# Kernel optimization log

Hardware: AMD Instinct MI355X
Metric: run time of the kernel (lower is better)

The kernel has to match this reference:

```python
import jax, jax.numpy as jnp
import numpy as np

H, W = 32, 64          # img_size
NB = 4                 # fno_blocks
SCALE = 0.02


def setup_inputs() -> dict:
    key = jax.random.key(0)
    ks = jax.random.split(key, 8)
    B, N, C = 16, H * W, 768
    BS = C // NB
    x = jax.random.normal(ks[0], (B, N, C), dtype=jnp.float32)
    w1 = SCALE * jax.random.normal(ks[1], (2, NB, BS, BS), dtype=jnp.float32)
    b1 = SCALE * jax.random.normal(ks[2], (2, NB, BS), dtype=jnp.float32)
    w2 = SCALE * jax.random.normal(ks[3], (2, NB, BS, BS), dtype=jnp.float32)
    b2 = SCALE * jax.random.normal(ks[4], (2, NB, BS), dtype=jnp.float32)
    # Conv1d(C, C, kernel_size=1) == per-token linear layer over channels
    bias_w = jax.random.normal(ks[5], (C, C), dtype=jnp.float32) / np.sqrt(C)
    bias_b = jax.random.normal(ks[6], (C,), dtype=jnp.float32) * 0.01
    return {"x": x, "w1": w1, "b1": b1, "w2": w2, "b2": b2,
            "bias_w": bias_w, "bias_b": bias_b}


def _mul(a, w):
    # block-diagonal matmul: a [..., NB, BS], w [NB, BS, BS]
    return jnp.einsum('...bd,bdk->...bk', a, w)


def reference(x, w1, b1, w2, b2, bias_w, bias_b):
    B, N, C = x.shape
    BS = C // NB
    # Conv1d kernel-size-1 bias path
    bias = x @ bias_w.T + bias_b
    # spatial FFT
    xf = jnp.fft.rfftn(x.reshape(B, H, W, C), axes=(1, 2), norm='ortho')
    xf = xf.reshape(B, H, W // 2 + 1, NB, BS)
    xr, xi = xf.real, xf.imag
    # layer 1 (complex block-diag matmul + bias, ReLU on real/imag separately)
    r1 = jax.nn.relu(_mul(xr, w1[0]) - _mul(xi, w1[1]) + b1[0])
    i1 = jax.nn.relu(_mul(xr, w1[1]) + _mul(xi, w1[0]) + b1[1])
    # layer 2 -- NOTE: imag part uses the *updated* real part, matching the
    # original torch code's in-place reassignment order.
    r2 = _mul(r1, w2[0]) - _mul(i1, w2[1]) + b2[0]
    i2 = _mul(r2, w2[1]) + _mul(i1, w2[0]) + b2[1]
    xc = jax.lax.complex(r2, i2).reshape(B, H, W // 2 + 1, C)
    out = jnp.fft.irfftn(xc, s=(H, W), axes=(1, 2), norm='ortho')
    return out.reshape(B, N, C) + bias
```

## Files before the change

kernel.cpp:

```cpp
#include <hip/hip_runtime.h>
#include <hip/hip_bf16.h>
#include <stdint.h>

#define BB 16
#define HH 32
#define WW 64
#define CC 768
#define W2C 33
#define ROWW (2*CC)

typedef __bf16 bf16x8 __attribute__((ext_vector_type(8)));
typedef float f32x4 __attribute__((ext_vector_type(4)));

__device__ __forceinline__ unsigned short f2bf(float f) {
  __hip_bfloat16 h = __float2bfloat16(f);
  return __builtin_bit_cast(unsigned short, h);
}
__device__ __forceinline__ float bf2f(unsigned short u) {
  union { unsigned int i; float f; } x;
  x.i = ((unsigned int)u) << 16;
  return x.f;
}

__device__ __forceinline__ void g2l16(const void* g, void* l) {
  __builtin_amdgcn_global_load_lds((const __attribute__((address_space(1))) unsigned int*)g,
                                   (__attribute__((address_space(3))) unsigned int*)l,
                                   16, 0, 0);
}

#define WAITVM(n) asm volatile("s_waitcnt vmcnt(" #n ")" ::: "memory")
#define LGKM0() asm volatile("s_waitcnt lgkmcnt(0)" ::: "memory")
#define MEMFENCE() asm volatile("" ::: "memory")

__device__ __host__ constexpr int brevc(int x, int bits) {
  int r = 0;
  for (int i = 0; i < bits; ++i) r |= ((x >> i) & 1) << (bits - 1 - i);
  return r;
}

constexpr double TPI = 6.283185307179586476925286766559;
constexpr double tsin_(double x) {
  double t = x, s = x, x2 = x * x;
  for (int i = 1; i < 14; ++i) { t *= -x2 / (double)((2 * i) * (2 * i + 1)); s += t; }
  return s;
}
constexpr double tcos_(double x) {
  double t = 1.0, s = 1.0, x2 = x * x;
  for (int i = 1; i < 14; ++i) { t *= -x2 / (double)((2 * i - 1) * (2 * i)); s += t; }
  return s;
}
struct Tw64 { float c[64]; float s[64]; };
constexpr Tw64 mk_tw() {
  Tw64 r{};
  for (int k = 0; k < 64; ++k) {
    int q = k >> 4, m = k & 15;
    double a = (TPI / 64.0) * m;
    double cq = tcos_(a), sq = tsin_(a);
    double c, s;
    if (q == 0)      { c =  cq; s =  sq; }
    else if (q == 1) { c = -sq; s =  cq; }
    else if (q == 2) { c = -cq; s = -sq; }
    else             { c =  sq; s = -cq; }
    r.c[k] = (float)c;
    r.s[k] = (float)(-s);
  }
  return r;
}
constexpr Tw64 TW = mk_tw();

template<int N, bool INV>
__device__ __forceinline__ void fft_reg(float2 (&v)[N]) {
  constexpr int LOG2N = (N == 64) ? 6 : 5;
#pragma unroll
  for (int s = 0; s < LOG2N; ++s) {
    const int len = N >> s;
    const int half = len >> 1;
    const int tstep = 64 / len;
#pragma unroll
    for (int i = 0; i < N; i += len) {
#pragma unroll
      for (int j = 0; j < half; ++j) {
        float2 u = v[i + j];
        float2 t = v[i + j + half];
        float sr = u.x + t.x, si = u.y + t.y;
        float dr = u.x - t.x, di = u.y - t.y;
        float wr = TW.c[j * tstep];
        float wi = INV ? -TW.s[j * tstep] : TW.s[j * tstep];
        v[i + j] = make_float2(sr, si);
        v[i + j + half] = make_float2(dr * wr - di * wi, dr * wi + di * wr);
      }
    }
  }
}

__global__ __launch_bounds__(128) void fft_fwd_w(const float* __restrict__ x,
                                                 ushort2* __restrict__ yw) {
  __shared__ __align__(16) float xs[32][128];
  const int t = threadIdx.x;
  const int bh = blockIdx.x;
  const int c0 = blockIdx.y * 128;
  const float* xrow = x + (size_t)bh * (WW * CC) + c0;
  const int rg = t >> 5;
  const int lc = (t & 31) * 4;
  float2 v[32];
#pragma unroll
  for (int half = 0; half < 2; ++half) {
    if (half) __syncthreads();
    float4 f[8];
#pragma unroll
    for (int it = 0; it < 8; ++it)
      f[it] = *(const float4*)(xrow + (size_t)(half * 32 + it * 4 + rg) * CC + lc);
#pragma unroll
    for (int it = 0; it < 8; ++it)
      *(float4*)&xs[it * 4 + rg][lc] = f[it];
    __syncthreads();
#pragma unroll
    for (int n = 0; n < 16; ++n)
      v[half * 16 + n] = make_float2(xs[2 * n][t], xs[2 * n + 1][t]);
  }
  fft_reg<32, false>(v);
  ushort2* yp = yw + (size_t)bh * (W2C * CC) + c0 + t;
  {
    float2 Z0 = v[0];
    yp[0] = make_ushort2(f2bf(Z0.x + Z0.y), f2bf(0.f));
    yp[(size_t)32 * CC] = make_ushort2(f2bf(Z0.x - Z0.y), f2bf(0.f));
  }
#pragma unroll
  for (int k = 1; k < 32; ++k) {
    float2 Zk = v[brevc(k, 5)];
    float2 Zm = v[brevc(32 - k, 5)];
    float Er = 0.5f * (Zk.x + Zm.x), Ei = 0.5f * (Zk.y - Zm.y);
    float Odr = 0.5f * (Zk.y + Zm.y), Odi = -0.5f * (Zk.x - Zm.x);
    float wx = TW.c[k], wy = TW.s[k];
    float Xr = Er + wx * Odr - wy * Odi;
    float Xi = Ei + wx * Odi + wy * Odr;
    yp[(size_t)k * CC] = make_ushort2(f2bf(Xr), f2bf(Xi));
  }
}

__global__ __launch_bounds__(256) void fft_fwd_h(const ushort2* __restrict__ yw,
                                                 unsigned short* __restrict__ xf) {
  const int bk = blockIdx.x;
  const int b = bk / W2C, kw = bk - b * W2C;
  const int c = blockIdx.y * 256 + threadIdx.x;
  const ushort2* yp = yw + ((size_t)b * HH * W2C + kw) * CC + c;
  float2 v[32];
#pragma unroll
  for (int h = 0; h < 32; ++h) {
    ushort2 u = yp[(size_t)h * (W2C * CC)];
    v[h] = make_float2(bf2f(u.x), bf2f(u.y));
  }
  fft_reg<32, false>(v);
  const int nb = c / 192, cc = c - nb * 192;
  ushort2* xp = (ushort2*)(xf + (size_t)nb * 384 + 2 * cc);
  const float s = 0.022097086912079608f;
#pragma unroll
  for (int kh = 0; kh < 32; ++kh) {
    float2 z = v[brevc(kh, 5)];
    size_t m = ((size_t)b * HH + kh) * W2C + kw;
    xp[m * (ROWW / 2)] = make_ushort2(f2bf(z.x * s), f2bf(z.y * s));
  }
}

__global__ __launch_bounds__(256) void fft_inv_h(const unsigned short* __restrict__ r2,
                                                 ushort2* __restrict__ g) {
  const int bk = blockIdx.x;
  const int b = bk / W2C, kw = bk - b * W2C;
  const int c = blockIdx.y * 256 + threadIdx.x;
  const int nb = c / 192, cc = c - nb * 192;
  const ushort2* rp = (const ushort2*)(r2 + (size_t)nb * 384 + 2 * cc);
  float2 v[32];
#pragma unroll
  for (int kh = 0; kh < 32; ++kh) {
    size_t m = ((size_t)b * HH + kh) * W2C + kw;
    ushort2 u = rp[m * (ROWW / 2)];
    v[kh] = make_float2(bf2f(u.x), bf2f(u.y));
  }
  fft_reg<32, true>(v);
  ushort2* gp = g + ((size_t)b * HH * W2C + kw) * CC + c;
#pragma unroll
  for (int h = 0; h < 32; ++h) {
    float2 z = v[brevc(h, 5)];
    gp[(size_t)h * (W2C * CC)] = make_ushort2(f2bf(z.x), f2bf(z.y));
  }
}

__global__ __launch_bounds__(128) void fft_inv_w(const ushort2* __restrict__ g,
                                                 const unsigned short* __restrict__ biasb,
                                                 float* __restrict__ out) {
  __shared__ __align__(16) float ys[32][128];
  const int t = threadIdx.x;
  const int bh = blockIdx.x;
  const int c0 = blockIdx.y * 128;
  const ushort2* gp = g + (size_t)bh * (W2C * CC) + c0 + t;
  float2 v[32];
  {
    float X0 = bf2f(gp[0].x);
    float X32 = bf2f(gp[(size_t)32 * CC].x);
    v[0] = make_float2(0.5f * (X0 + X32), 0.5f * (X0 - X32));
  }
#pragma unroll
  for (int k = 1; k < 32; ++k) {
    ushort2 uk = gp[(size_t)k * CC];
    ushort2 um = gp[(size_t)(32 - k) * CC];
    float2 Xk = make_float2(bf2f(uk.x), bf2f(uk.y));
    float2 Xm = make_float2(bf2f(um.x), bf2f(um.y));
    float Ar = 0.5f * (Xk.x + Xm.x), Ai = 0.5f * (Xk.y - Xm.y);
    float Dr = 0.5f * (Xk.x - Xm.x), Di = 0.5f * (Xk.y + Xm.y);
    float wx = TW.c[k], wy = TW.s[k];
    float Br = wx * Dr + wy * Di;
    float Bi = wx * Di - wy * Dr;
    v[k] = make_float2(Ar - Bi, Ai + Br);
  }
  fft_reg<32, true>(v);
  const float s2 = 0.04419417382415922f;
  float* orow = out + (size_t)bh * (WW * CC) + c0;
  const unsigned short* brow = biasb + (size_t)bh * (WW * CC) + c0;
  const int rg = t >> 5;
  const int lc = (t & 31) * 4;
#pragma unroll
  for (int half = 0; half < 2; ++half) {
    if (half) __syncthreads();
    ushort4 b4[8];
#pragma unroll
    for (int it = 0; it < 8; ++it)
      b4[it] = *(const ushort4*)(brow + (size_t)(half * 32 + it * 4 + rg) * CC + lc);
#pragma unroll
    for (int n = 0; n < 16; ++n) {
      float2 z = v[brevc(half * 16 + n, 5)];
      ys[2 * n][t] = z.x * s2;
      ys[2 * n + 1][t] = z.y * s2;
    }
    __syncthreads();
#pragma unroll
    for (int it = 0; it < 8; ++it) {
      const int w = half * 32 + it * 4 + rg;
      float4 f = *(const float4*)&ys[it * 4 + rg][lc];
      f.x += bf2f(b4[it].x); f.y += bf2f(b4[it].y);
      f.z += bf2f(b4[it].z); f.w += bf2f(b4[it].w);
      *(float4*)(orow + (size_t)w * CC + lc) = f;
    }
  }
}

template<bool RELU, bool OBF>
__global__ __launch_bounds__(256) void gemm_bt(
    const unsigned short* __restrict__ A, int lda, int aZ,
    const unsigned short* __restrict__ Bw, int K, int bZ,
    const float* __restrict__ bias, int biasZ,
    void* __restrict__ outp, int ldo, int oZ) {
  __shared__ __align__(16) unsigned short As[2][128 * 32];
  __shared__ __align__(16) unsigned short Bs[2][128 * 32];
  const int t = threadIdx.x;
  const int z = blockIdx.z;
  const size_t m0 = (size_t)blockIdx.x * 128;
  const int n0 = blockIdx.y * 128;
  const unsigned short* Ap = A + m0 * lda + (size_t)z * aZ;
  const unsigned short* Bp = Bw + (size_t)n0 * K + (size_t)z * bZ;
  const int lane = t & 63, wave = t >> 6;
  const int lr = lane & 15, quad = lane >> 4;
  const int wm = (wave >> 1) * 64, wn = (wave & 1) * 64;
  const int row = t >> 2;
  const int sl = t & 3;
  const int kb = (sl ^ ((row >> 1) & 3)) * 8;
  const int swzf = (lr >> 1) & 3;
  const int NT = K >> 5;
  f32x4 acc[4][4] = {};

#define STG(k0_, s_) do { \
    const unsigned short* ga_ = Ap + (size_t)row * lda + ((k0_) + kb); \
    g2l16(ga_, &As[s_][row * 32 + sl * 8]); \
    g2l16(ga_ + (size_t)64 * lda, &As[s_][(row + 64) * 32 + sl * 8]); \
    const unsigned short* gb_ = Bp + (size_t)row * K + ((k0_) + kb); \
    g2l16(gb_, &Bs[s_][row * 32 + sl * 8]); \
    g2l16(gb_ + (size_t)64 * K, &Bs[s_][(row + 64) * 32 + sl * 8]); \
  } while (0)

  STG(0, 0);
  WAITVM(0);
  MEMFENCE(); __builtin_amdgcn_s_barrier(); MEMFENCE();
  int cur = 0;
  for (int tt = 0; tt < NT; ++tt) {
    if (tt + 1 < NT) STG((tt + 1) * 32, cur ^ 1);
    bf16x8 af[4], bfr[4];
#pragma unroll
    for (int mi = 0; mi < 4; ++mi)
      af[mi] = *(const bf16x8*)&As[cur][(wm + mi * 16 + lr) * 32 + ((quad ^ swzf) * 8)];
#pragma unroll
    for (int ni = 0; ni < 4; ++ni)
      bfr[ni] = *(const bf16x8*)&Bs[cur][(wn + ni * 16 + lr) * 32 + ((quad ^ swzf) * 8)];
    __builtin_amdgcn_s_setprio(1);
#pragma unroll
    for (int mi = 0; mi < 4; ++mi)
#pragma unroll
      for (int ni = 0; ni < 4; ++ni)
        acc[mi][ni] = __builtin_amdgcn_mfma_f32_16x16x32_bf16(af[mi], bfr[ni], acc[mi][ni], 0, 0, 0);
    __builtin_amdgcn_s_setprio(0);
    if (tt + 1 < NT) {
      WAITVM(0);
      MEMFENCE(); __builtin_amdgcn_s_barrier(); MEMFENCE();
      cur ^= 1;
    }
  }
#undef STG

#pragma unroll
  for (int mi = 0; mi < 4; ++mi) {
    const size_t mrow = m0 + wm + mi * 16 + quad * 4;
#pragma unroll
    for (int ni = 0; ni < 4; ++ni) {
      const int ncol = n0 + wn + ni * 16 + lr;
      const float bv = bias[z * biasZ + ncol];
#pragma unroll
      for (int r = 0; r < 4; ++r) {
        float vv = acc[mi][ni][r] + bv;
        if (RELU) vv = fmaxf(vv, 0.f);
        const size_t off = (mrow + r) * (size_t)ldo + (size_t)z * oZ + ncol;
        if (OBF) ((unsigned short*)outp)[off] = f2bf(vv);
        else ((float*)outp)[off] = vv;
      }
    }
  }
}

__global__ __launch_bounds__(256) void gemm_bias(
    const float* __restrict__ A,
    const unsigned short* __restrict__ Bw,
    const float* __restrict__ bias,
    unsigned short* __restrict__ outp) {
  constexpr int K = 768, NT = 24, LDAF = 768;
  __shared__ __align__(16) unsigned short As[2][128 * 32];
  __shared__ __align__(16) unsigned short Bs[2][128 * 32];
  const int t = threadIdx.x;
  const size_t m0 = (size_t)blockIdx.x * 128;
  const int n0 = blockIdx.y * 128;
  const float* Ap = A + m0 * LDAF;
  const unsigned short* Bp = Bw + (size_t)n0 * K;
  const int lane = t & 63, wave = t >> 6;
  const int lr = lane & 15, quad = lane >> 4;
  const int wm = (wave >> 1) * 64, wn = (wave & 1) * 64;
  const int row = t >> 2, sl = t & 3;
  const int kb = (sl ^ ((row >> 1) & 3)) * 8;
  const int swzf = (lr >> 1) & 3;
  f32x4 acc[4][4] = {};
  float4 a0, a1, a2, a3;

#define LDA4(k0_) do { \
    const float* ga_ = Ap + (size_t)row * LDAF + ((k0_) + kb); \
    a0 = *(const float4*)ga_; a1 = *(const float4*)(ga_ + 4); \
    const float* gc_ = ga_ + (size_t)64 * LDAF; \
    a2 = *(const float4*)gc_; a3 = *(const float4*)(gc_ + 4); \
  } while (0)
#define STB(k0_, s_) do { \
    const unsigned short* gb_ = Bp + (size_t)row * K + ((k0_) + kb); \
    g2l16(gb_, &Bs[s_][row * 32 + sl * 8]); \
    g2l16(gb_ + (size_t)64 * K, &Bs[s_][(row + 64) * 32 + sl * 8]); \
  } while (0)
#define WRA(s_) do { \
    union { bf16x8 v; unsigned short u[8]; } p0_, p1_; \
    p0_.u[0] = f2bf(a0.x); p0_.u[1] = f2bf(a0.y); p0_.u[2] = f2bf(a0.z); p0_.u[3] = f2bf(a0.w); \
    p0_.u[4] = f2bf(a1.x); p0_.u[5] = f2bf(a1.y); p0_.u[6] = f2bf(a1.z); p0_.u[7] = f2bf(a1.w); \
    p1_.u[0] = f2bf(a2.x); p1_.u[1] = f2bf(a2.y); p1_.u[2] = f2bf(a2.z); p1_.u[3] = f2bf(a2.w); \
    p1_.u[4] = f2bf(a3.x); p1_.u[5] = f2bf(a3.y); p1_.u[6] = f2bf(a3.z); p1_.u[7] = f2bf(a3.w); \
    *(bf16x8*)&As[s_][row * 32 + sl * 8] = p0_.v; \
    *(bf16x8*)&As[s_][(row + 64) * 32 + sl * 8] = p1_.v; \
  } while (0)

  LDA4(0); STB(0, 0);
  WRA(0);
  WAITVM(0); LGKM0();
  MEMFENCE(); __builtin_amdgcn_s_barrier(); MEMFENCE();
  int cur = 0;
  for (int tt = 0; tt < NT; ++tt) {
    if (tt + 1 < NT) { LDA4((tt + 1) * 32); STB((tt + 1) * 32, cur ^ 1); }
    bf16x8 af[4], bfr[4];
#pragma unroll
    for (int mi = 0; mi < 4; ++mi)
      af[mi] = *(const bf16x8*)&As[cur][(wm + mi * 16 + lr) * 32 + ((quad ^ swzf) * 8)];
#pragma unroll
    for (int ni = 0; ni < 4; ++ni)
      bfr[ni] = *(const bf16x8*)&Bs[cur][(wn + ni * 16 + lr) * 32 + ((quad ^ swzf) * 8)];
    __builtin_amdgcn_s_setprio(1);
#pragma unroll
    for (int mi = 0; mi < 4; ++mi)
#pragma unroll
      for (int ni = 0; ni < 4; ++ni)
        acc[mi][ni] = __builtin_amdgcn_mfma_f32_16x16x32_bf16(af[mi], bfr[ni], acc[mi][ni], 0, 0, 0);
    __builtin_amdgcn_s_setprio(0);
    if (tt + 1 < NT) {
      WRA(cur ^ 1);
      WAITVM(0); LGKM0();
      MEMFENCE(); __builtin_amdgcn_s_barrier(); MEMFENCE();
      cur ^= 1;
    }
  }
#undef LDA4
#undef STB
#undef WRA

#pragma unroll
  for (int mi = 0; mi < 4; ++mi) {
    const size_t mrow = m0 + wm + mi * 16 + quad * 4;
#pragma unroll
    for (int ni = 0; ni < 4; ++ni) {
      const int ncol = n0 + wn + ni * 16 + lr;
      const float bv = bias[ncol];
#pragma unroll
      for (int r = 0; r < 4; ++r)
        outp[(mrow + r) * (size_t)768 + ncol] = f2bf(acc[mi][ni][r] + bv);
    }
  }
}

__global__ __launch_bounds__(256) void cvt_bf16(const float* __restrict__ in,
                                                unsigned short* __restrict__ outp) {
  const size_t i = ((size_t)blockIdx.x * 256 + threadIdx.x) * 4;
  float4 v = *(const float4*)(in + i);
  ushort4 o = make_ushort4(f2bf(v.x), f2bf(v.y), f2bf(v.z), f2bf(v.w));
  *(ushort4*)(outp + i) = o;
}

__global__ __launch_bounds__(256) void build_w1(const float* __restrict__ w1,
                                                const float* __restrict__ b1,
                                                unsigned short* __restrict__ w1t,
                                                float* __restrict__ bias1) {
  const int idx = blockIdx.x * 256 + threadIdx.x;
  const int nb = idx / (384 * 384);
  const int rem = idx - nb * (384 * 384);
  const int n = rem / 384, k = rem - (rem / 384) * 384;
  const bool khi = k >= 192, nhi = n >= 192;
  const int kk = khi ? k - 192 : k, nn = nhi ? n - 192 : n;
  float val;
  if (!khi && !nhi)      val =  w1[((0 * 4 + nb) * 192 + kk) * 192 + nn];
  else if (khi && !nhi)  val = -w1[((1 * 4 + nb) * 192 + kk) * 192 + nn];
  else if (!khi && nhi)  val =  w1[((1 * 4 + nb) * 192 + kk) * 192 + nn];
  else                   val =  w1[((0 * 4 + nb) * 192 + kk) * 192 + nn];
  const int k2 = 2 * kk + (khi ? 1 : 0);
  const int n2 = 2 * nn + (nhi ? 1 : 0);
  w1t[((size_t)nb * 384 + n2) * 384 + k2] = f2bf(val);
  if (k == 0)
    bias1[nb * 384 + n2] = nhi ? b1[(1 * 4 + nb) * 192 + nn] : b1[(0 * 4 + nb) * 192 + nn];
}

__global__ __launch_bounds__(256) void build_w2(const float* __restrict__ w2,
                                                const float* __restrict__ b2,
                                                unsigned short* __restrict__ w2t,
                                                float* __restrict__ bias2) {
  const int idx = blockIdx.x * 256 + threadIdx.x;
  const int nb = idx / (384 * 384);
  const int rem = idx - nb * (384 * 384);
  const int k = rem / 384, n = rem - (rem / 384) * 384;
  const bool khi = k >= 192, nhi = n >= 192;
  const int kk = khi ? k - 192 : k, nn = nhi ? n - 192 : n;
  float val;
  if (!khi && !nhi) {
    val = w2[((0 * 4 + nb) * 192 + kk) * 192 + nn];
  } else if (khi && !nhi) {
    val = -w2[((1 * 4 + nb) * 192 + kk) * 192 + nn];
  } else if (!khi && nhi) {
    float s = 0.f;
    for (int d = 0; d < 192; ++d)
      s += w2[((0 * 4 + nb) * 192 + kk) * 192 + d] * w2[((1 * 4 + nb) * 192 + d) * 192 + nn];
    val = s;
  } else {
    float s = 0.f;
    for (int d = 0; d < 192; ++d)
      s += w2[((1 * 4 + nb) * 192 + kk) * 192 + d] * w2[((1 * 4 + nb) * 192 + d) * 192 + nn];
    val = w2[((0 * 4 + nb) * 192 + kk) * 192 + nn] - s;
  }
  const int k2 = 2 * kk + (khi ? 1 : 0);
  const int n2 = 2 * nn + (nhi ? 1 : 0);
  w2t[((size_t)nb * 384 + n2) * 384 + k2] = f2bf(val);
  if (k == 0) {
    float bv;
    if (!nhi) {
      bv = b2[(0 * 4 + nb) * 192 + nn];
    } else {
      float s = 0.f;
      for (int d = 0; d < 192; ++d)
        s += b2[(0 * 4 + nb) * 192 + d] * w2[((1 * 4 + nb) * 192 + d) * 192 + nn];
      bv = b2[(1 * 4 + nb) * 192 + nn] + s;
    }
    bias2[nb * 384 + n2] = bv;
  }
}

extern "C" void kernel_launch(void* const* d_in, const int* in_sizes, int n_in,
                              void* d_out, int out_size, void* d_ws, size_t ws_size,
                              hipStream_t stream) {
  (void)in_sizes; (void)n_in; (void)out_size; (void)ws_size;
  const float* x  = (const float*)d_in[0];
  const float* w1 = (const float*)d_in[1];
  const float* b1 = (const float*)d_in[2];
  const float* w2 = (const float*)d_in[3];
  const float* b2 = (const float*)d_in[4];
  const float* bw = (const float*)d_in[5];
  const float* bb = (const float*)d_in[6];
  float* out = (float*)d_out;

  char* p = (char*)d_ws;
  unsigned short* buf1 = (unsigned short*)p; p += 51904512;
  unsigned short* buf2 = (unsigned short*)p; p += 51904512;
  unsigned short* buf3 = (unsigned short*)p; p += 51904512;
  unsigned short* bwb  = (unsigned short*)p; p += 1179648;
  unsigned short* w1t  = (unsigned short*)p; p += 1179648;
  unsigned short* w2t  = (unsigned short*)p; p += 1179648;
  float* bias1 = (float*)p; p += 6144;
  float* bias2 = (float*)p; p += 6144;

  cvt_bf16<<<589824 / 1024, 256, 0, stream>>>(bw, bwb);
  build_w1<<<589824 / 256, 256, 0, stream>>>(w1, b1, w1t, bias1);
  build_w2<<<589824 / 256, 256, 0, stream>>>(w2, b2, w2t, bias2);
  fft_fwd_w<<<dim3(BB * HH, 6), 128, 0, stream>>>(x, (ushort2*)buf1);
  gemm_bias<<<dim3(256, 6), 256, 0, stream>>>(x, bwb, bb, buf3);
  fft_fwd_h<<<dim3(BB * W2C, 3), 256, 0, stream>>>((const ushort2*)buf1, buf2);
  gemm_bt<true, true><<<dim3(132, 3, 4), 256, 0, stream>>>(
      buf2, ROWW, 384, w1t, 384, 384 * 384, bias1, 384, buf1, ROWW, 384);
  gemm_bt<false, true><<<dim3(132, 3, 4), 256, 0, stream>>>(
      buf1, ROWW, 384, w2t, 384, 384 * 384, bias2, 384, buf2, ROWW, 384);
  fft_inv_h<<<dim3(BB * W2C, 3), 256, 0, stream>>>(buf2, (ushort2*)buf1);
  fft_inv_w<<<dim3(BB * HH, 6), 128, 0, stream>>>((const ushort2*)buf1, buf3, out);
}
```

Before: 438.1 us.

## Merge weight prep kernels and co-schedule bias GEMM with forward H-FFT

The three weight-preparation kernels are merged into one launch that dispatches on block index. The bias-path GEMM and the forward H-direction FFT are combined into a single heterogeneous kernel that interleaves GEMM tiles with FFT blocks, so compute-bound MFMA work and memory-bound FFT work can share the GPU concurrently. This cuts launch count and inter-kernel gaps. In exchange the FFT blocks now reserve the GEMM's shared memory and register budget, which may lower their occupancy.

```diff
diff --git a/kernel.cpp b/kernel.cpp
--- a/kernel.cpp
+++ b/kernel.cpp
@@ -138,27 +138,121 @@
   }
 }
 
-__global__ __launch_bounds__(256) void fft_fwd_h(const ushort2* __restrict__ yw,
-                                                 unsigned short* __restrict__ xf) {
-  const int bk = blockIdx.x;
-  const int b = bk / W2C, kw = bk - b * W2C;
-  const int c = blockIdx.y * 256 + threadIdx.x;
-  const ushort2* yp = yw + ((size_t)b * HH * W2C + kw) * CC + c;
-  float2 v[32];
-#pragma unroll
-  for (int h = 0; h < 32; ++h) {
-    ushort2 u = yp[(size_t)h * (W2C * CC)];
-    v[h] = make_float2(bf2f(u.x), bf2f(u.y));
-  }
-  fft_reg<32, false>(v);
-  const int nb = c / 192, cc = c - nb * 192;
-  ushort2* xp = (ushort2*)(xf + (size_t)nb * 384 + 2 * cc);
-  const float s = 0.022097086912079608f;
-#pragma unroll
-  for (int kh = 0; kh < 32; ++kh) {
-    float2 z = v[brevc(kh, 5)];
-    size_t m = ((size_t)b * HH + kh) * W2C + kw;
-    xp[m * (ROWW / 2)] = make_ushort2(f2bf(z.x * s), f2bf(z.y * s));
+__global__ __launch_bounds__(256) void fused_bias_ffth(
+    const float* __restrict__ x, const unsigned short* __restrict__ bwb,
+    const float* __restrict__ bb, unsigned short* __restrict__ biasout,
+    const ushort2* __restrict__ yw, unsigned short* __restrict__ xf) {
+  __shared__ __align__(16) unsigned short As[2][128 * 32];
+  __shared__ __align__(16) unsigned short Bs[2][128 * 32];
+  const int gid = blockIdx.x;
+  bool isg; int idx;
+  if (gid < 3072) { isg = (gid & 1) == 0; idx = gid >> 1; }
+  else            { isg = false; idx = 1536 + (gid - 3072); }
+
+  if (isg) {
+    constexpr int K = 768, NT = 24, LDAF = 768;
+    const int t = threadIdx.x;
+    const int bx = idx & 255, by = idx >> 8;
+    const size_t m0 = (size_t)bx * 128;
+    const int n0 = by * 128;
+    const float* Ap = x + m0 * LDAF;
+    const unsigned short* Bp = bwb + (size_t)n0 * K;
+    const int lane = t & 63, wave = t >> 6;
+    const int lr = lane & 15, quad = lane >> 4;
+    const int wm = (wave >> 1) * 64, wn = (wave & 1) * 64;
+    const int row = t >> 2, sl = t & 3;
+    const int kb = (sl ^ ((row >> 1) & 3)) * 8;
+    const int swzf = (lr >> 1) & 3;
+    f32x4 acc[4][4] = {};
+    float4 a0, a1, a2, a3;
+
+#define LDA4(k0_) do { \
+    const float* ga_ = Ap + (size_t)row * LDAF + ((k0_) + kb); \
+    a0 = *(const float4*)ga_; a1 = *(const float4*)(ga_ + 4); \
+    const float* gc_ = ga_ + (size_t)64 * LDAF; \
+    a2 = *(const float4*)gc_; a3 = *(const float4*)(gc_ + 4); \
+  } while (0)
+#define STB(k0_, s_) do { \
+    const unsigned short* gb_ = Bp + (size_t)row * K + ((k0_) + kb); \
+    g2l16(gb_, &Bs[s_][row * 32 + sl * 8]); \
+    g2l16(gb_ + (size_t)64 * K, &Bs[s_][(row + 64) * 32 + sl * 8]); \
+  } while (0)
+#define WRA(s_) do { \
+    union { bf16x8 v; unsigned short u[8]; } p0_, p1_; \
+    p0_.u[0] = f2bf(a0.x); p0_.u[1] = f2bf(a0.y); p0_.u[2] = f2bf(a0.z); p0_.u[3] = f2bf(a0.w); \
+    p0_.u[4] = f2bf(a1.x); p0_.u[5] = f2bf(a1.y); p0_.u[6] = f2bf(a1.z); p0_.u[7] = f2bf(a1.w); \
+    p1_.u[0] = f2bf(a2.x); p1_.u[1] = f2bf(a2.y); p1_.u[2] = f2bf(a2.z); p1_.u[3] = f2bf(a2.w); \
+    p1_.u[4] = f2bf(a3.x); p1_.u[5] = f2bf(a3.y); p1_.u[6] = f2bf(a3.z); p1_.u[7] = f2bf(a3.w); \
+    *(bf16x8*)&As[s_][row * 32 + sl * 8] = p0_.v; \
+    *(bf16x8*)&As[s_][(row + 64) * 32 + sl * 8] = p1_.v; \
+  } while (0)
+
+    LDA4(0); STB(0, 0);
+    WRA(0);
+    WAITVM(0); LGKM0();
+    MEMFENCE(); __builtin_amdgcn_s_barrier(); MEMFENCE();
+    int cur = 0;
+    for (int tt = 0; tt < NT; ++tt) {
+      if (tt + 1 < NT) { LDA4((tt + 1) * 32); STB((tt + 1) * 32, cur ^ 1); }
+      bf16x8 af[4], bfr[4];
+#pragma unroll
+      for (int mi = 0; mi < 4; ++mi)
+        af[mi] = *(const bf16x8*)&As[cur][(wm + mi * 16 + lr) * 32 + ((quad ^ swzf) * 8)];
+#pragma unroll
+      for (int ni = 0; ni < 4; ++ni)
+        bfr[ni] = *(const bf16x8*)&Bs[cur][(wn + ni * 16 + lr) * 32 + ((quad ^ swzf) * 8)];
+      __builtin_amdgcn_s_setprio(1);
+#pragma unroll
+      for (int mi = 0; mi < 4; ++mi)
+#pragma unroll
+        for (int ni = 0; ni < 4; ++ni)
+          acc[mi][ni] = __builtin_amdgcn_mfma_f32_16x16x32_bf16(af[mi], bfr[ni], acc[mi][ni], 0, 0, 0);
+      __builtin_amdgcn_s_setprio(0);
+      if (tt + 1 < NT) {
+        WRA(cur ^ 1);
+        WAITVM(0); LGKM0();
+        MEMFENCE(); __builtin_amdgcn_s_barrier(); MEMFENCE();
+        cur ^= 1;
+      }
+    }
+#undef LDA4
+#undef STB
+#undef WRA
+
+#pragma unroll
+    for (int mi = 0; mi < 4; ++mi) {
+      const size_t mrow = m0 + wm + mi * 16 + quad * 4;
+#pragma unroll
+      for (int ni = 0; ni < 4; ++ni) {
+        const int ncol = n0 + wn + ni * 16 + lr;
+        const float bv = bb[ncol];
+#pragma unroll
+        for (int r = 0; r < 4; ++r)
+          biasout[(mrow + r) * (size_t)768 + ncol] = f2bf(acc[mi][ni][r] + bv);
+      }
+    }
+  } else {
+    const int bk = idx - (idx / 528) * 528;
+    const int cy = idx / 528;
+    const int b = bk / W2C, kw = bk - b * W2C;
+    const int c = cy * 256 + threadIdx.x;
+    const ushort2* yp = yw + ((size_t)b * HH * W2C + kw) * CC + c;
+    float2 v[32];
+#pragma unroll
+    for (int h = 0; h < 32; ++h) {
+      ushort2 u = yp[(size_t)h * (W2C * CC)];
+      v[h] = make_float2(bf2f(u.x), bf2f(u.y));
+    }
+    fft_reg<32, false>(v);
+    const int nb = c / 192, cc = c - nb * 192;
+    ushort2* xp = (ushort2*)(xf + (size_t)nb * 384 + 2 * cc);
+    const float s = 0.022097086912079608f;
+#pragma unroll
+    for (int kh = 0; kh < 32; ++kh) {
+      float2 z = v[brevc(kh, 5)];
+      size_t m = ((size_t)b * HH + kh) * W2C + kw;
+      xp[m * (ROWW / 2)] = make_ushort2(f2bf(z.x * s), f2bf(z.y * s));
+    }
   }
 }
 
@@ -323,165 +417,73 @@
   }
 }
 
-__global__ __launch_bounds__(256) void gemm_bias(
-    const float* __restrict__ A,
-    const unsigned short* __restrict__ Bw,
-    const float* __restrict__ bias,
-    unsigned short* __restrict__ outp) {
-  constexpr int K = 768, NT = 24, LDAF = 768;
-  __shared__ __align__(16) unsigned short As[2][128 * 32];
-  __shared__ __align__(16) unsigned short Bs[2][128 * 32];
+__global__ __launch_bounds__(256) void prep_all(
+    const float* __restrict__ bw, unsigned short* __restrict__ bwb,
+    const float* __restrict__ w1, const float* __restrict__ b1,
+    unsigned short* __restrict__ w1t, float* __restrict__ bias1,
+    const float* __restrict__ w2, const float* __restrict__ b2,
+    unsigned short* __restrict__ w2t, float* __restrict__ bias2) {
+  const int gid = blockIdx.x;
   const int t = threadIdx.x;
-  const size_t m0 = (size_t)blockIdx.x * 128;
-  const int n0 = blockIdx.y * 128;
-  const float* Ap = A + m0 * LDAF;
-  const unsigned short* Bp = Bw + (size_t)n0 * K;
-  const int lane = t & 63, wave = t >> 6;
-  const int lr = lane & 15, quad = lane >> 4;
-  const int wm = (wave >> 1) * 64, wn = (wave & 1) * 64;
-  const int row = t >> 2, sl = t & 3;
-  const int kb = (sl ^ ((row >> 1) & 3)) * 8;
-  const int swzf = (lr >> 1) & 3;
-  f32x4 acc[4][4] = {};
-  float4 a0, a1, a2, a3;
-
-#define LDA4(k0_) do { \
-    const float* ga_ = Ap + (size_t)row * LDAF + ((k0_) + kb); \
-    a0 = *(const float4*)ga_; a1 = *(const float4*)(ga_ + 4); \
-    const float* gc_ = ga_ + (size_t)64 * LDAF; \
-    a2 = *(const float4*)gc_; a3 = *(const float4*)(gc_ + 4); \
-  } while (0)
-#define STB(k0_, s_) do { \
-    const unsigned short* gb_ = Bp + (size_t)row * K + ((k0_) + kb); \
-    g2l16(gb_, &Bs[s_][row * 32 + sl * 8]); \
-    g2l16(gb_ + (size_t)64 * K, &Bs[s_][(row + 64) * 32 + sl * 8]); \
-  } while (0)
-#define WRA(s_) do { \
-    union { bf16x8 v; unsigned short u[8]; } p0_, p1_; \
-    p0_.u[0] = f2bf(a0.x); p0_.u[1] = f2bf(a0.y); p0_.u[2] = f2bf(a0.z); p0_.u[3] = f2bf(a0.w); \
-    p0_.u[4] = f2bf(a1.x); p0_.u[5] = f2bf(a1.y); p0_.u[6] = f2bf(a1.z); p0_.u[7] = f2bf(a1.w); \
-    p1_.u[0] = f2bf(a2.x); p1_.u[1] = f2bf(a2.y); p1_.u[2] = f2bf(a2.z); p1_.u[3] = f2bf(a2.w); \
-    p1_.u[4] = f2bf(a3.x); p1_.u[5] = f2bf(a3.y); p1_.u[6] = f2bf(a3.z); p1_.u[7] = f2bf(a3.w); \
-    *(bf16x8*)&As[s_][row * 32 + sl * 8] = p0_.v; \
-    *(bf16x8*)&As[s_][(row + 64) * 32 + sl * 8] = p1_.v; \
-  } while (0)
-
-  LDA4(0); STB(0, 0);
-  WRA(0);
-  WAITVM(0); LGKM0();
-  MEMFENCE(); __builtin_amdgcn_s_barrier(); MEMFENCE();
-  int cur = 0;
-  for (int tt = 0; tt < NT; ++tt) {
-    if (tt + 1 < NT) { LDA4((tt + 1) * 32); STB((tt + 1) * 32, cur ^ 1); }
-    bf16x8 af[4], bfr[4];
-#pragma unroll
-    for (int mi = 0; mi < 4; ++mi)
-      af[mi] = *(const bf16x8*)&As[cur][(wm + mi * 16 + lr) * 32 + ((quad ^ swzf) * 8)];
-#pragma unroll
-    for (int ni = 0; ni < 4; ++ni)
-      bfr[ni] = *(const bf16x8*)&Bs[cur][(wn + ni * 16 + lr) * 32 + ((quad ^ swzf) * 8)];
-    __builtin_amdgcn_s_setprio(1);
-#pragma unroll
-    for (int mi = 0; mi < 4; ++mi)
-#pragma unroll
-      for (int ni = 0; ni < 4; ++ni)
-        acc[mi][ni] = __builtin_amdgcn_mfma_f32_16x16x32_bf16(af[mi], bfr[ni], acc[mi][ni], 0, 0, 0);
-    __builtin_amdgcn_s_setprio(0);
-    if (tt + 1 < NT) {
-      WRA(cur ^ 1);
-      WAITVM(0); LGKM0();
-      MEMFENCE(); __builtin_amdgcn_s_barrier(); MEMFENCE();
-      cur ^= 1;
-    }
-  }
-#undef LDA4
-#undef STB
-#undef WRA
-
-#pragma unroll
-  for (int mi = 0; mi < 4; ++mi) {
-    const size_t mrow = m0 + wm + mi * 16 + quad * 4;
-#pragma unroll
-    for (int ni = 0; ni < 4; ++ni) {
-      const int ncol = n0 + wn + ni * 16 + lr;
-      const float bv = bias[ncol];
-#pragma unroll
-      for (int r = 0; r < 4; ++r)
-        outp[(mrow + r) * (size_t)768 + ncol] = f2bf(acc[mi][ni][r] + bv);
-    }
-  }
-}
-
-__global__ __launch_bounds__(256) void cvt_bf16(const float* __restrict__ in,
-                                                unsigned short* __restrict__ outp) {
-  const size_t i = ((size_t)blockIdx.x * 256 + threadIdx.x) * 4;
-  float4 v = *(const float4*)(in + i);
-  ushort4 o = make_ushort4(f2bf(v.x), f2bf(v.y), f2bf(v.z), f2bf(v.w));
-  *(ushort4*)(outp + i) = o;
-}
-
-__global__ __launch_bounds__(256) void build_w1(const float* __restrict__ w1,
-                                                const float* __restrict__ b1,
-                                                unsigned short* __restrict__ w1t,
-                                                float* __restrict__ bias1) {
-  const int idx = blockIdx.x * 256 + threadIdx.x;
-  const int nb = idx / (384 * 384);
-  const int rem = idx - nb * (384 * 384);
-  const int n = rem / 384, k = rem - (rem / 384) * 384;
-  const bool khi = k >= 192, nhi = n >= 192;
-  const int kk = khi ? k - 192 : k, nn = nhi ? n - 192 : n;
-  float val;
-  if (!khi && !nhi)      val =  w1[((0 * 4 + nb) * 192 + kk) * 192 + nn];
-  else if (khi && !nhi)  val = -w1[((1 * 4 + nb) * 192 + kk) * 192 + nn];
-  else if (!khi && nhi)  val =  w1[((1 * 4 + nb) * 192 + kk) * 192 + nn];
-  else                   val =  w1[((0 * 4 + nb) * 192 + kk) * 192 + nn];
-  const int k2 = 2 * kk + (khi ? 1 : 0);
-  const int n2 = 2 * nn + (nhi ? 1 : 0);
-  w1t[((size_t)nb * 384 + n2) * 384 + k2] = f2bf(val);
-  if (k == 0)
-    bias1[nb * 384 + n2] = nhi ? b1[(1 * 4 + nb) * 192 + nn] : b1[(0 * 4 + nb) * 192 + nn];
-}
-
-__global__ __launch_bounds__(256) void build_w2(const float* __restrict__ w2,
-                                                const float* __restrict__ b2,
-                                                unsigned short* __restrict__ w2t,
-                                                float* __restrict__ bias2) {
-  const int idx = blockIdx.x * 256 + threadIdx.x;
-  const int nb = idx / (384 * 384);
-  const int rem = idx - nb * (384 * 384);
-  const int k = rem / 384, n = rem - (rem / 384) * 384;
-  const bool khi = k >= 192, nhi = n >= 192;
-  const int kk = khi ? k - 192 : k, nn = nhi ? n - 192 : n;
-  float val;
-  if (!khi && !nhi) {
-    val = w2[((0 * 4 + nb) * 192 + kk) * 192 + nn];
-  } else if (khi && !nhi) {
-    val = -w2[((1 * 4 + nb) * 192 + kk) * 192 + nn];
-  } else if (!khi && nhi) {
-    float s = 0.f;
-    for (int d = 0; d < 192; ++d)
-      s += w2[((0 * 4 + nb) * 192 + kk) * 192 + d] * w2[((1 * 4 + nb) * 192 + d) * 192 + nn];
-    val = s;
+  if (gid < 576) {
+    const size_t i = ((size_t)gid * 256 + t) * 4;
+    float4 v = *(const float4*)(bw + i);
+    *(ushort4*)(bwb + i) = make_ushort4(f2bf(v.x), f2bf(v.y), f2bf(v.z), f2bf(v.w));
+  } else if (gid < 576 + 2304) {
+    const int idx = (gid - 576) * 256 + t;
+    const int nb = idx / (384 * 384);
+    const int rem = idx - nb * (384 * 384);
+    const int n = rem / 384, k = rem - (rem / 384) * 384;
+    const bool khi = k >= 192, nhi = n >= 192;
+    const int kk = khi ? k - 192 : k, nn = nhi ? n - 192 : n;
+    float val;
+    if (!khi && !nhi)      val =  w1[((0 * 4 + nb) * 192 + kk) * 192 + nn];
+    else if (khi && !nhi)  val = -w1[((1 * 4 + nb) * 192 + kk) * 192 + nn];
+    else if (!khi && nhi)  val =  w1[((1 * 4 + nb) * 192 + kk) * 192 + nn];
+    else                   val =  w1[((0 * 4 + nb) * 192 + kk) * 192 + nn];
+    const int k2 = 2 * kk + (khi ? 1 : 0);
+    const int n2 = 2 * nn + (nhi ? 1 : 0);
+    w1t[((size_t)nb * 384 + n2) * 384 + k2] = f2bf(val);
+    if (k == 0)
+      bias1[nb * 384 + n2] = nhi ? b1[(1 * 4 + nb) * 192 + nn] : b1[(0 * 4 + nb) * 192 + nn];
   } else {
-    float s = 0.f;
-    for (int d = 0; d < 192; ++d)
-      s += w2[((1 * 4 + nb) * 192 + kk) * 192 + d] * w2[((1 * 4 + nb) * 192 + d) * 192 + nn];
-    val = w2[((0 * 4 + nb) * 192 + kk) * 192 + nn] - s;
-  }
-  const int k2 = 2 * kk + (khi ? 1 : 0);
-  const int n2 = 2 * nn + (nhi ? 1 : 0);
-  w2t[((size_t)nb * 384 + n2) * 384 + k2] = f2bf(val);
-  if (k == 0) {
-    float bv;
-    if (!nhi) {
-      bv = b2[(0 * 4 + nb) * 192 + nn];
+    const int idx = (gid - 2880) * 256 + t;
+    const int nb = idx / (384 * 384);
+    const int rem = idx - nb * (384 * 384);
+    const int k = rem / 384, n = rem - (rem / 384) * 384;
+    const bool khi = k >= 192, nhi = n >= 192;
+    const int kk = khi ? k - 192 : k, nn = nhi ? n - 192 : n;
+    float val;
+    if (!khi && !nhi) {
+      val = w2[((0 * 4 + nb) * 192 + kk) * 192 + nn];
+    } else if (khi && !nhi) {
+      val = -w2[((1 * 4 + nb) * 192 + kk) * 192 + nn];
+    } else if (!khi && nhi) {
+      float s = 0.f;
+      for (int d = 0; d < 192; ++d)
+        s += w2[((0 * 4 + nb) * 192 + kk) * 192 + d] * w2[((1 * 4 + nb) * 192 + d) * 192 + nn];
+      val = s;
     } else {
       float s = 0.f;
       for (int d = 0; d < 192; ++d)
-        s += b2[(0 * 4 + nb) * 192 + d] * w2[((1 * 4 + nb) * 192 + d) * 192 + nn];
-      bv = b2[(1 * 4 + nb) * 192 + nn] + s;
-    }
-    bias2[nb * 384 + n2] = bv;
+        s += w2[((1 * 4 + nb) * 192 + kk) * 192 + d] * w2[((1 * 4 + nb) * 192 + d) * 192 + nn];
+      val = w2[((0 * 4 + nb) * 192 + kk) * 192 + nn] - s;
+    }
+    const int k2 = 2 * kk + (khi ? 1 : 0);
+    const int n2 = 2 * nn + (nhi ? 1 : 0);
+    w2t[((size_t)nb * 384 + n2) * 384 + k2] = f2bf(val);
+    if (k == 0) {
+      float bv;
+      if (!nhi) {
+        bv = b2[(0 * 4 + nb) * 192 + nn];
+      } else {
+        float s = 0.f;
+        for (int d = 0; d < 192; ++d)
+          s += b2[(0 * 4 + nb) * 192 + d] * w2[((1 * 4 + nb) * 192 + d) * 192 + nn];
+        bv = b2[(1 * 4 + nb) * 192 + nn] + s;
+      }
+      bias2[nb * 384 + n2] = bv;
+    }
   }
 }
 
@@ -508,12 +510,9 @@
   float* bias1 = (float*)p; p += 6144;
   float* bias2 = (float*)p; p += 6144;
 
-  cvt_bf16<<<589824 / 1024, 256, 0, stream>>>(bw, bwb);
-  build_w1<<<589824 / 256, 256, 0, stream>>>(w1, b1, w1t, bias1);
-  build_w2<<<589824 / 256, 256, 0, stream>>>(w2, b2, w2t, bias2);
+  prep_all<<<5184, 256, 0, stream>>>(bw, bwb, w1, b1, w1t, bias1, w2, b2, w2t, bias2);
   fft_fwd_w<<<dim3(BB * HH, 6), 128, 0, stream>>>(x, (ushort2*)buf1);
-  gemm_bias<<<dim3(256, 6), 256, 0, stream>>>(x, bwb, bb, buf3);
-  fft_fwd_h<<<dim3(BB * W2C, 3), 256, 0, stream>>>((const ushort2*)buf1, buf2);
+  fused_bias_ffth<<<3120, 256, 0, stream>>>(x, bwb, bb, buf3, (const ushort2*)buf1, buf2);
   gemm_bt<true, true><<<dim3(132, 3, 4), 256, 0, stream>>>(
       buf2, ROWW, 384, w1t, 384, 384 * 384, bias1, 384, buf1, ROWW, 384);
   gemm_bt<false, true><<<dim3(132, 3, 4), 256, 0, stream>>>(
```

New measurement: 500.2 us. 1.14x slower.
